# Performance work log

Measured on AMD Instinct MI355X. Metric: run time of the kernel, lower is better.

## Reference

```python
import jax, jax.numpy as jnp
import numpy as np

TEMPERATURE = 1.0
NUM_EXPERTS = 8


def setup_inputs() -> dict:
    key = jax.random.key(0)
    ks = jax.random.split(key, 7)
    B, S, H, E = 4, 4096, 1024, NUM_EXPERTS
    scale = 1.0 / np.sqrt(H)
    return {
        "hidden_states": jax.random.normal(ks[0], (B, S, H), dtype=jnp.float32),
        "w1": jax.random.normal(ks[1], (H, H // 2), dtype=jnp.float32) * scale,
        "b1": jax.random.normal(ks[2], (H // 2,), dtype=jnp.float32) * 0.01,
        "w2": jax.random.normal(ks[3], (H // 2, E), dtype=jnp.float32) * (1.0 / np.sqrt(H // 2)),
        "b2": jax.random.normal(ks[4], (E,), dtype=jnp.float32) * 0.01,
        "expert_W": jax.random.normal(ks[5], (E, H, H), dtype=jnp.float32) * scale,
        "expert_b": jax.random.normal(ks[6], (E, H), dtype=jnp.float32) * 0.01,
    }


def reference(hidden_states, w1, b1, w2, b2, expert_W, expert_b):
    # Router MLP: Linear(H, H//2) -> ReLU -> Linear(H//2, E)  (dropout inactive at eval)
    h = jax.nn.relu(jnp.einsum("bsh,hm->bsm", hidden_states, w1) + b1)
    routing_scores = (jnp.einsum("bsm,me->bse", h, w2) + b2) / TEMPERATURE
    expert_probs = jax.nn.softmax(routing_scores, axis=-1)
    # top-1 routing (topk with k=1 == argmax of probs)
    top_idx = jnp.argmax(expert_probs, axis=-1)  # [B, S]
    onehot = jax.nn.one_hot(top_idx, NUM_EXPERTS, dtype=hidden_states.dtype)  # [B, S, E]

    # _apply_expert_routing: for each expert, masked input -> dense transform -> masked accumulate
    routed = jnp.zeros_like(hidden_states)
    for e in range(NUM_EXPERTS):
        mask = onehot[..., e:e + 1]  # [B, S, 1]
        expert_out = jnp.einsum("bsh,hd->bsd", hidden_states * mask, expert_W[e]) + expert_b[e]
        routed = routed + expert_out * mask
    return routed
```

## Files before the change

### kernel.cpp

```cpp
#include <hip/hip_runtime.h>

#define NTOK 16384
#define HDIM 1024
#define MDIM 512
#define NEXP 8
#define CHUNK 128
#define MAXCHUNK 136
#define RCAP 4096
#define DELTA 0.02f
#define LSTR 72

typedef __bf16 bf16x8 __attribute__((ext_vector_type(8)));
typedef float floatx4 __attribute__((ext_vector_type(4)));

__global__ __launch_bounds__(256) void cvt_hs(
    const float* __restrict__ src, __bf16* __restrict__ dst)
{
  const size_t i = ((size_t)blockIdx.x * 256 + threadIdx.x) * 8;
  float4 a = *(const float4*)&src[i];
  float4 b = *(const float4*)&src[i + 4];
  bf16x8 o;
  o[0] = (__bf16)a.x; o[1] = (__bf16)a.y; o[2] = (__bf16)a.z; o[3] = (__bf16)a.w;
  o[4] = (__bf16)b.x; o[5] = (__bf16)b.y; o[6] = (__bf16)b.z; o[7] = (__bf16)b.w;
  *(bf16x8*)&dst[i] = o;
}

__global__ __launch_bounds__(256) void transpose_cvt(
    const float* __restrict__ src, __bf16* __restrict__ dst, int K, int C)
{
  __shared__ __align__(16) __bf16 T[64 * LSTR];
  const int b = blockIdx.z;
  const int k0 = blockIdx.x * 64, c0 = blockIdx.y * 64;
  const float* S = src + (size_t)b * K * C;
  __bf16* D = dst + (size_t)b * K * C;
  const int t = threadIdx.x;

  {
    const int r = t >> 2, cc = (t & 3) * 16;
    const float* p = S + (size_t)(k0 + r) * C + c0 + cc;
    float4 v0 = *(const float4*)&p[0];
    float4 v1 = *(const float4*)&p[4];
    float4 v2 = *(const float4*)&p[8];
    float4 v3 = *(const float4*)&p[12];
    float vv[16] = {v0.x, v0.y, v0.z, v0.w, v1.x, v1.y, v1.z, v1.w,
                    v2.x, v2.y, v2.z, v2.w, v3.x, v3.y, v3.z, v3.w};
#pragma unroll
    for (int j = 0; j < 16; ++j) T[(cc + j) * LSTR + r] = (__bf16)vv[j];
  }
  __syncthreads();
  {
    const int c = t >> 2, kk = (t & 3) * 16;
    __bf16* q = D + (size_t)(c0 + c) * K + k0 + kk;
    *(float4*)&q[0] = *(const float4*)&T[c * LSTR + kk];
    *(float4*)&q[8] = *(const float4*)&T[c * LSTR + kk + 8];
  }
}

__global__ __launch_bounds__(256) void gemm1_v2(
    const __bf16* __restrict__ A,
    const __bf16* __restrict__ Bt,
    const float* __restrict__ bias,
    float* __restrict__ Hout)
{
  __shared__ __align__(16) __bf16 As[128 * LSTR];
  __shared__ __align__(16) __bf16 Bs[128 * LSTR];

  const int tid = threadIdx.x;
  const int row0 = blockIdx.y * 128, col0 = blockIdx.x * 128;

  const int srow = tid >> 3;
  const int soff = (tid & 7) * 8;

  const __bf16* pa = A + (size_t)(row0 + srow) * HDIM + soff;
  const __bf16* pb = Bt + (size_t)(col0 + srow) * HDIM + soff;

  const int wave = tid >> 6, lane = tid & 63;
  const int wr = (wave >> 1) * 64, wc = (wave & 1) * 64;
  const int lrow = lane & 15, quad = lane >> 4;

  floatx4 acc[4][4];
#pragma unroll
  for (int i = 0; i < 4; ++i)
#pragma unroll
    for (int j = 0; j < 4; ++j) acc[i][j] = (floatx4){0.f, 0.f, 0.f, 0.f};

  for (int k0 = 0; k0 < HDIM; k0 += 64) {
#pragma unroll
    for (int p = 0; p < 4; ++p) {
      *(float4*)&As[(srow + p * 32) * LSTR + soff] =
          *(const float4*)&pa[(size_t)(p * 32) * HDIM + k0];
      *(float4*)&Bs[(srow + p * 32) * LSTR + soff] =
          *(const float4*)&pb[(size_t)(p * 32) * HDIM + k0];
    }
    __syncthreads();

#pragma unroll
    for (int kh = 0; kh < 2; ++kh) {
      bf16x8 a[4], b[4];
#pragma unroll
      for (int i = 0; i < 4; ++i)
        a[i] = *(const bf16x8*)&As[(wr + i * 16 + lrow) * LSTR + kh * 32 + quad * 8];
#pragma unroll
      for (int j = 0; j < 4; ++j)
        b[j] = *(const bf16x8*)&Bs[(wc + j * 16 + lrow) * LSTR + kh * 32 + quad * 8];
#pragma unroll
      for (int i = 0; i < 4; ++i)
#pragma unroll
        for (int j = 0; j < 4; ++j)
          acc[i][j] = __builtin_amdgcn_mfma_f32_16x16x32_bf16(a[i], b[j], acc[i][j], 0, 0, 0);
    }
    __syncthreads();
  }

#pragma unroll
  for (int i = 0; i < 4; ++i)
#pragma unroll
    for (int r = 0; r < 4; ++r) {
      const int row = row0 + wr + i * 16 + quad * 4 + r;
#pragma unroll
      for (int j = 0; j < 4; ++j) {
        const int col = col0 + wc + j * 16 + lrow;
        Hout[(size_t)row * MDIM + col] = fmaxf(acc[i][j][r] + bias[col], 0.f);
      }
    }
}

__global__ __launch_bounds__(256) void routing_flag(
    const float* __restrict__ Hq, const float* __restrict__ w2,
    const float* __restrict__ b2, int* __restrict__ top_idx,
    int* __restrict__ risky_n, int* __restrict__ risky)
{
  __shared__ int rbuf[4];
  __shared__ int rcnt;
  if (threadIdx.x == 0) rcnt = 0;
  __syncthreads();

  const int warp = threadIdx.x >> 6;
  const int lane = threadIdx.x & 63;
  const int t = blockIdx.x * 4 + warp;
  const float* hrow = Hq + (size_t)t * MDIM;

  float s[8] = {0, 0, 0, 0, 0, 0, 0, 0};
  for (int k = lane; k < MDIM; k += 64) {
    float hv = hrow[k];
    float4 wa = *(const float4*)&w2[k * 8];
    float4 wb = *(const float4*)&w2[k * 8 + 4];
    s[0] += hv * wa.x; s[1] += hv * wa.y; s[2] += hv * wa.z; s[3] += hv * wa.w;
    s[4] += hv * wb.x; s[5] += hv * wb.y; s[6] += hv * wb.z; s[7] += hv * wb.w;
  }
#pragma unroll
  for (int off = 32; off > 0; off >>= 1)
#pragma unroll
    for (int e = 0; e < 8; ++e) s[e] += __shfl_xor(s[e], off, 64);

  if (lane == 0) {
    float best = s[0] + b2[0], second = -1e30f;
    int bi = 0;
#pragma unroll
    for (int e = 1; e < 8; ++e) {
      float v = s[e] + b2[e];
      if (v > best) { second = best; best = v; bi = e; }
      else if (v > second) second = v;
    }
    top_idx[t] = bi;
    if (best - second < DELTA) {
      int slot = atomicAdd(&rcnt, 1);
      rbuf[slot] = t;
    }
  }
  __syncthreads();
  if (threadIdx.x == 0 && rcnt > 0) {
    int base = atomicAdd(risky_n, rcnt);
    for (int i = 0; i < rcnt; ++i)
      if (base + i < RCAP) risky[base + i] = rbuf[i];
  }
}

__global__ __launch_bounds__(256) void gemm1_fix_v2(
    const float* __restrict__ A,
    const float* __restrict__ W,
    const float* __restrict__ bias,
    const int* __restrict__ risky,
    float* __restrict__ Hout)
{
  __shared__ float As[32][33];
  __shared__ float Bs[32][64];
  __shared__ int toks[32];

  const int tid = threadIdx.x;
  if (tid < 32) toks[tid] = risky[blockIdx.y * 32 + tid];
  __syncthreads();
  if (toks[0] < 0) return;

  const int col0 = blockIdx.x * 64;
  const int tx = tid & 15, ty = tid >> 4;

  float acc0[4] = {0, 0, 0, 0}, acc1[4] = {0, 0, 0, 0};

  const int sr = tid >> 3;
  const int sc4 = (tid & 7) * 4;
  const int sc8 = (tid & 7) * 8;
  const int tokS = toks[sr];
  const float* pa = (tokS >= 0) ? A + (size_t)tokS * HDIM + sc4 : A;

  for (int k0 = 0; k0 < HDIM; k0 += 32) {
    float4 av = (tokS >= 0) ? *(const float4*)&pa[k0] : make_float4(0, 0, 0, 0);
    float4 b0 = *(const float4*)&W[(size_t)(k0 + sr) * MDIM + col0 + sc8];
    float4 b1v = *(const float4*)&W[(size_t)(k0 + sr) * MDIM + col0 + sc8 + 4];
    As[sc4 + 0][sr] = av.x; As[sc4 + 1][sr] = av.y;
    As[sc4 + 2][sr] = av.z; As[sc4 + 3][sr] = av.w;
    *(float4*)&Bs[sr][sc8] = b0;
    *(float4*)&Bs[sr][sc8 + 4] = b1v;
    __syncthreads();

#pragma unroll
    for (int k = 0; k < 32; ++k) {
      float a0 = As[k][ty], a1 = As[k][ty + 16];
      float4 bv = *(const float4*)&Bs[k][tx * 4];
      acc0[0] = fmaf(a0, bv.x, acc0[0]); acc0[1] = fmaf(a0, bv.y, acc0[1]);
      acc0[2] = fmaf(a0, bv.z, acc0[2]); acc0[3] = fmaf(a0, bv.w, acc0[3]);
      acc1[0] = fmaf(a1, bv.x, acc1[0]); acc1[1] = fmaf(a1, bv.y, acc1[1]);
      acc1[2] = fmaf(a1, bv.z, acc1[2]); acc1[3] = fmaf(a1, bv.w, acc1[3]);
    }
    __syncthreads();
  }

  const int c = col0 + tx * 4;
  const int t0 = toks[ty], t1 = toks[ty + 16];
  if (t0 >= 0) {
    float4 v;
    v.x = fmaxf(acc0[0] + bias[c + 0], 0.f); v.y = fmaxf(acc0[1] + bias[c + 1], 0.f);
    v.z = fmaxf(acc0[2] + bias[c + 2], 0.f); v.w = fmaxf(acc0[3] + bias[c + 3], 0.f);
    *(float4*)&Hout[(size_t)t0 * MDIM + c] = v;
  }
  if (t1 >= 0) {
    float4 v;
    v.x = fmaxf(acc1[0] + bias[c + 0], 0.f); v.y = fmaxf(acc1[1] + bias[c + 1], 0.f);
    v.z = fmaxf(acc1[2] + bias[c + 2], 0.f); v.w = fmaxf(acc1[3] + bias[c + 3], 0.f);
    *(float4*)&Hout[(size_t)t1 * MDIM + c] = v;
  }
}

__global__ __launch_bounds__(256) void rescore_fix(
    const float* __restrict__ Hq, const float* __restrict__ w2,
    const float* __restrict__ b2, const int* __restrict__ risky,
    int* __restrict__ top_idx)
{
  const int idx = blockIdx.x * 32 + (threadIdx.x >> 3);
  const int l8 = threadIdx.x & 7;
  const int t = risky[idx];

  float s[8] = {0, 0, 0, 0, 0, 0, 0, 0};
  if (t >= 0) {
    const float* hrow = Hq + (size_t)t * MDIM;
    for (int k = l8; k < MDIM; k += 8) {
      float hv = hrow[k];
      float4 wa = *(const float4*)&w2[k * 8];
      float4 wb = *(const float4*)&w2[k * 8 + 4];
      s[0] += hv * wa.x; s[1] += hv * wa.y; s[2] += hv * wa.z; s[3] += hv * wa.w;
      s[4] += hv * wb.x; s[5] += hv * wb.y; s[6] += hv * wb.z; s[7] += hv * wb.w;
    }
  }
#pragma unroll
  for (int off = 4; off > 0; off >>= 1)
#pragma unroll
    for (int e = 0; e < 8; ++e) s[e] += __shfl_xor(s[e], off, 64);

  if (l8 == 0 && t >= 0) {
    float best = s[0] + b2[0];
    int bi = 0;
#pragma unroll
    for (int e = 1; e < 8; ++e) {
      float v = s[e] + b2[e];
      if (v > best) { best = v; bi = e; }
    }
    top_idx[t] = bi;
  }
}

__global__ __launch_bounds__(256) void count_tokens(
    const int* __restrict__ top_idx, int* __restrict__ counts)
{
  __shared__ int lc[NEXP];
  if (threadIdx.x < NEXP) lc[threadIdx.x] = 0;
  __syncthreads();
  const int t = blockIdx.x * 256 + threadIdx.x;
  atomicAdd(&lc[top_idx[t]], 1);
  __syncthreads();
  if (threadIdx.x < NEXP) atomicAdd(&counts[threadIdx.x], lc[threadIdx.x]);
}

__global__ void make_offsets(const int* __restrict__ counts,
                             int* __restrict__ pad_off)
{
  if (threadIdx.x == 0) {
    int off = 0;
    for (int e = 0; e < NEXP; ++e) {
      pad_off[e] = off;
      off += ((counts[e] + CHUNK - 1) / CHUNK) * CHUNK;
    }
    pad_off[NEXP] = off;
  }
}

__global__ __launch_bounds__(256) void scatter_tokens(
    const int* __restrict__ top_idx, const int* __restrict__ pad_off,
    int* __restrict__ cursor, int* __restrict__ sorted)
{
  __shared__ int lc[NEXP];
  __shared__ int lbase[NEXP];
  if (threadIdx.x < NEXP) lc[threadIdx.x] = 0;
  __syncthreads();
  const int t = blockIdx.x * 256 + threadIdx.x;
  const int e = top_idx[t];
  const int r = atomicAdd(&lc[e], 1);
  __syncthreads();
  if (threadIdx.x < NEXP)
    lbase[threadIdx.x] = atomicAdd(&cursor[threadIdx.x], lc[threadIdx.x]);
  __syncthreads();
  sorted[pad_off[e] + lbase[e] + r] = t;
}

__global__ __launch_bounds__(256) void expert_gemm_v2(
    const __bf16* __restrict__ A,
    const __bf16* __restrict__ Wt,
    const float* __restrict__ Eb,
    const int* __restrict__ sorted,
    const int* __restrict__ top_idx,
    float* __restrict__ Out)
{
  __shared__ __align__(16) __bf16 As[128 * LSTR];
  __shared__ __align__(16) __bf16 Bs[128 * LSTR];
  __shared__ int toks[CHUNK];

  const int tid = threadIdx.x;
  if (tid < CHUNK) toks[tid] = sorted[(size_t)blockIdx.y * CHUNK + tid];
  __syncthreads();
  if (toks[0] < 0) return;

  const int e = top_idx[toks[0]];
  const int col0 = blockIdx.x * 128;

  const int srow = tid >> 3;
  const int soff = (tid & 7) * 8;

  const __bf16* pa[4];
#pragma unroll
  for (int p = 0; p < 4; ++p) {
    int tk = toks[srow + p * 32];
    pa[p] = A + (size_t)(tk >= 0 ? tk : 0) * HDIM + soff;
  }
  const __bf16* pb = Wt + ((size_t)e * HDIM + col0 + srow) * HDIM + soff;

  const int wave = tid >> 6, lane = tid & 63;
  const int wr = (wave >> 1) * 64, wc = (wave & 1) * 64;
  const int lrow = lane & 15, quad = lane >> 4;

  floatx4 acc[4][4];
#pragma unroll
  for (int i = 0; i < 4; ++i)
#pragma unroll
    for (int j = 0; j < 4; ++j) acc[i][j] = (floatx4){0.f, 0.f, 0.f, 0.f};

  for (int k0 = 0; k0 < HDIM; k0 += 64) {
#pragma unroll
    for (int p = 0; p < 4; ++p) {
      *(float4*)&As[(srow + p * 32) * LSTR + soff] = *(const float4*)&pa[p][k0];
      *(float4*)&Bs[(srow + p * 32) * LSTR + soff] =
          *(const float4*)&pb[(size_t)(p * 32) * HDIM + k0];
    }
    __syncthreads();

#pragma unroll
    for (int kh = 0; kh < 2; ++kh) {
      bf16x8 a[4], b[4];
#pragma unroll
      for (int i = 0; i < 4; ++i)
        a[i] = *(const bf16x8*)&As[(wr + i * 16 + lrow) * LSTR + kh * 32 + quad * 8];
#pragma unroll
      for (int j = 0; j < 4; ++j)
        b[j] = *(const bf16x8*)&Bs[(wc + j * 16 + lrow) * LSTR + kh * 32 + quad * 8];
#pragma unroll
      for (int i = 0; i < 4; ++i)
#pragma unroll
        for (int j = 0; j < 4; ++j)
          acc[i][j] = __builtin_amdgcn_mfma_f32_16x16x32_bf16(a[i], b[j], acc[i][j], 0, 0, 0);
    }
    __syncthreads();
  }

  const float* be = Eb + (size_t)e * HDIM + col0;
#pragma unroll
  for (int i = 0; i < 4; ++i)
#pragma unroll
    for (int r = 0; r < 4; ++r) {
      const int row = wr + i * 16 + quad * 4 + r;
      const int tok = toks[row];
      if (tok < 0) continue;
      float* po = Out + (size_t)tok * HDIM + col0;
#pragma unroll
      for (int j = 0; j < 4; ++j) {
        const int col = wc + j * 16 + lrow;
        po[col] = acc[i][j][r] + be[col];
      }
    }
}

extern "C" void kernel_launch(void* const* d_in, const int* in_sizes, int n_in,
                              void* d_out, int out_size, void* d_ws, size_t ws_size,
                              hipStream_t stream) {
  (void)in_sizes; (void)n_in; (void)out_size; (void)ws_size;

  const float* hs = (const float*)d_in[0];
  const float* w1 = (const float*)d_in[1];
  const float* b1 = (const float*)d_in[2];
  const float* w2 = (const float*)d_in[3];
  const float* b2 = (const float*)d_in[4];
  const float* eW = (const float*)d_in[5];
  const float* eb = (const float*)d_in[6];
  float* out = (float*)d_out;

  float* h = (float*)d_out;

  char* wsb = (char*)d_ws;
  int* top_idx = (int*)wsb;
  int* ctrl    = (int*)(wsb + 65536);
  int* counts  = ctrl;
  int* risky_n = ctrl + 8;
  int* cursor  = ctrl + 16;
  int* pad_off = (int*)(wsb + 65536 + 128);
  int* risky   = (int*)(wsb + 65792);
  int* sorted  = risky + RCAP;
  __bf16* hs_bf = (__bf16*)(wsb + 163840);
  __bf16* w1t   = (__bf16*)(wsb + 163840 + 33554432);
  __bf16* eWt   = (__bf16*)(wsb + 163840 + 33554432 + 1048576);

  hipMemsetAsync(ctrl, 0, 128, stream);
  hipMemsetAsync(risky, 0xFF, (RCAP + MAXCHUNK * CHUNK) * sizeof(int), stream);

  cvt_hs<<<NTOK * HDIM / (256 * 8), 256, 0, stream>>>(hs, hs_bf);
  transpose_cvt<<<dim3(HDIM / 64, MDIM / 64, 1), 256, 0, stream>>>(w1, w1t, HDIM, MDIM);
  transpose_cvt<<<dim3(HDIM / 64, HDIM / 64, NEXP), 256, 0, stream>>>(eW, eWt, HDIM, HDIM);

  gemm1_v2<<<dim3(MDIM / 128, NTOK / 128), 256, 0, stream>>>(hs_bf, w1t, b1, h);
  routing_flag<<<NTOK / 4, 256, 0, stream>>>(h, w2, b2, top_idx, risky_n, risky);
  gemm1_fix_v2<<<dim3(MDIM / 64, RCAP / 32), 256, 0, stream>>>(hs, w1, b1, risky, h);
  rescore_fix<<<RCAP / 32, 256, 0, stream>>>(h, w2, b2, risky, top_idx);
  count_tokens<<<NTOK / 256, 256, 0, stream>>>(top_idx, counts);
  make_offsets<<<1, 64, 0, stream>>>(counts, pad_off);
  scatter_tokens<<<NTOK / 256, 256, 0, stream>>>(top_idx, pad_off, cursor, sorted);
  expert_gemm_v2<<<dim3(HDIM / 128, MAXCHUNK), 256, 0, stream>>>(hs_bf, eWt, eb, sorted, top_idx, out);
}
```

Measured before the change: 340.6 us.

## Fuse router score into GEMM1 epilogue and use direct global-to-LDS swizzled loads

Router GEMM1 now computes the second linear layer (w2 projection) in its epilogue and writes per-column-block partial scores, so the 16384x512 hidden activation is no longer stored and reread. A separate argmax kernel reduces the partial scores and flags near-tie tokens. Recomputed hidden rows for flagged tokens go to a compact buffer. Both bf16 GEMMs switch to global_load_lds 16-byte loads with an XOR-swizzled unpadded LDS layout to cut VGPR staging and bank conflicts. make_offsets is folded into scatter_tokens, removing one launch. The fused epilogue adds shuffle reductions and an extra LDS pass.

```diff
diff --git a/kernel.cpp b/kernel.cpp
--- a/kernel.cpp
+++ b/kernel.cpp
@@ -13,6 +13,12 @@
 typedef __bf16 bf16x8 __attribute__((ext_vector_type(8)));
 typedef float floatx4 __attribute__((ext_vector_type(4)));
 
+__device__ __forceinline__ void gll16(const void* g, void* l) {
+  __builtin_amdgcn_global_load_lds(
+      (const __attribute__((address_space(1))) void*)g,
+      (__attribute__((address_space(3))) void*)l, 16, 0, 0);
+}
+
 __global__ __launch_bounds__(256) void cvt_hs(
     const float* __restrict__ src, __bf16* __restrict__ dst)
 {
@@ -34,7 +40,6 @@
   const float* S = src + (size_t)b * K * C;
   __bf16* D = dst + (size_t)b * K * C;
   const int t = threadIdx.x;
-
   {
     const int r = t >> 2, cc = (t & 3) * 16;
     const float* p = S + (size_t)(k0 + r) * C + c0 + cc;
@@ -56,28 +61,32 @@
   }
 }
 
-__global__ __launch_bounds__(256) void gemm1_v2(
+__global__ __launch_bounds__(256) void gemm1_score(
     const __bf16* __restrict__ A,
     const __bf16* __restrict__ Bt,
     const float* __restrict__ bias,
-    float* __restrict__ Hout)
-{
-  __shared__ __align__(16) __bf16 As[128 * LSTR];
-  __shared__ __align__(16) __bf16 Bs[128 * LSTR];
+    const float* __restrict__ w2,
+    float* __restrict__ scores_part)
+{
+  __shared__ __align__(16) __bf16 As[128 * 64];
+  __shared__ __align__(16) __bf16 Bs[128 * 64];
 
   const int tid = threadIdx.x;
   const int row0 = blockIdx.y * 128, col0 = blockIdx.x * 128;
-
-  const int srow = tid >> 3;
-  const int soff = (tid & 7) * 8;
-
-  const __bf16* pa = A + (size_t)(row0 + srow) * HDIM + soff;
-  const __bf16* pb = Bt + (size_t)(col0 + srow) * HDIM + soff;
-
   const int wave = tid >> 6, lane = tid & 63;
+  const int lrow8 = lane >> 3;
+  const int gchunk = (lane & 7) ^ lrow8;
   const int wr = (wave >> 1) * 64, wc = (wave & 1) * 64;
   const int lrow = lane & 15, quad = lane >> 4;
 
+  const __bf16 *pa[4], *pb[4];
+#pragma unroll
+  for (int p = 0; p < 4; ++p) {
+    const int rb = wave * 8 + p * 32;
+    pa[p] = A + (size_t)(row0 + rb + lrow8) * HDIM + gchunk * 8;
+    pb[p] = Bt + (size_t)(col0 + rb + lrow8) * HDIM + gchunk * 8;
+  }
+
   floatx4 acc[4][4];
 #pragma unroll
   for (int i = 0; i < 4; ++i)
@@ -87,22 +96,22 @@
   for (int k0 = 0; k0 < HDIM; k0 += 64) {
 #pragma unroll
     for (int p = 0; p < 4; ++p) {
-      *(float4*)&As[(srow + p * 32) * LSTR + soff] =
-          *(const float4*)&pa[(size_t)(p * 32) * HDIM + k0];
-      *(float4*)&Bs[(srow + p * 32) * LSTR + soff] =
-          *(const float4*)&pb[(size_t)(p * 32) * HDIM + k0];
-    }
-    __syncthreads();
-
+      const int rb = wave * 8 + p * 32;
+      gll16(pa[p] + k0, &As[rb * 64]);
+      gll16(pb[p] + k0, &Bs[rb * 64]);
+    }
+    __syncthreads();
 #pragma unroll
     for (int kh = 0; kh < 2; ++kh) {
       bf16x8 a[4], b[4];
 #pragma unroll
       for (int i = 0; i < 4; ++i)
-        a[i] = *(const bf16x8*)&As[(wr + i * 16 + lrow) * LSTR + kh * 32 + quad * 8];
+        a[i] = *(const bf16x8*)&As[(wr + i * 16 + lrow) * 64 +
+                                   (((kh * 4 + quad) ^ (lrow & 7)) * 8)];
 #pragma unroll
       for (int j = 0; j < 4; ++j)
-        b[j] = *(const bf16x8*)&Bs[(wc + j * 16 + lrow) * LSTR + kh * 32 + quad * 8];
+        b[j] = *(const bf16x8*)&Bs[(wc + j * 16 + lrow) * 64 +
+                                   (((kh * 4 + quad) ^ (lrow & 7)) * 8)];
 #pragma unroll
       for (int i = 0; i < 4; ++i)
 #pragma unroll
@@ -112,76 +121,101 @@
     __syncthreads();
   }
 
-#pragma unroll
-  for (int i = 0; i < 4; ++i)
+  float* w2s = (float*)As;
+  float* sblk = (float*)Bs;
+  *(float4*)&w2s[tid * 4] = *(const float4*)&w2[col0 * 8 + tid * 4];
+  __syncthreads();
+
+  float bj[4];
+  float4 wja[4], wjb[4];
+#pragma unroll
+  for (int j = 0; j < 4; ++j) {
+    const int cl = wc + j * 16 + lrow;
+    bj[j] = bias[col0 + cl];
+    wja[j] = *(const float4*)&w2s[cl * 8];
+    wjb[j] = *(const float4*)&w2s[cl * 8 + 4];
+  }
+
+#pragma unroll
+  for (int i = 0; i < 4; ++i) {
 #pragma unroll
     for (int r = 0; r < 4; ++r) {
-      const int row = row0 + wr + i * 16 + quad * 4 + r;
+      float4 sA = {0, 0, 0, 0}, sB = {0, 0, 0, 0};
 #pragma unroll
       for (int j = 0; j < 4; ++j) {
-        const int col = col0 + wc + j * 16 + lrow;
-        Hout[(size_t)row * MDIM + col] = fmaxf(acc[i][j][r] + bias[col], 0.f);
+        float h = fmaxf(acc[i][j][r] + bj[j], 0.f);
+        sA.x += h * wja[j].x; sA.y += h * wja[j].y;
+        sA.z += h * wja[j].z; sA.w += h * wja[j].w;
+        sB.x += h * wjb[j].x; sB.y += h * wjb[j].y;
+        sB.z += h * wjb[j].z; sB.w += h * wjb[j].w;
       }
-    }
-}
-
-__global__ __launch_bounds__(256) void routing_flag(
-    const float* __restrict__ Hq, const float* __restrict__ w2,
-    const float* __restrict__ b2, int* __restrict__ top_idx,
-    int* __restrict__ risky_n, int* __restrict__ risky)
-{
-  __shared__ int rbuf[4];
-  __shared__ int rcnt;
+#pragma unroll
+      for (int m = 1; m <= 8; m <<= 1) {
+        sA.x += __shfl_xor(sA.x, m, 64); sA.y += __shfl_xor(sA.y, m, 64);
+        sA.z += __shfl_xor(sA.z, m, 64); sA.w += __shfl_xor(sA.w, m, 64);
+        sB.x += __shfl_xor(sB.x, m, 64); sB.y += __shfl_xor(sB.y, m, 64);
+        sB.z += __shfl_xor(sB.z, m, 64); sB.w += __shfl_xor(sB.w, m, 64);
+      }
+      if (lrow == 0) {
+        const int rloc = wr + i * 16 + quad * 4 + r;
+        *(float4*)&sblk[((wave & 1) * 128 + rloc) * 8] = sA;
+        *(float4*)&sblk[((wave & 1) * 128 + rloc) * 8 + 4] = sB;
+      }
+    }
+  }
+  __syncthreads();
+  {
+    const int r = tid >> 1, e4 = (tid & 1) * 4;
+    float4 v0 = *(const float4*)&sblk[r * 8 + e4];
+    float4 v1 = *(const float4*)&sblk[(128 + r) * 8 + e4];
+    float4 o = {v0.x + v1.x, v0.y + v1.y, v0.z + v1.z, v0.w + v1.w};
+    *(float4*)&scores_part[((size_t)blockIdx.x * NTOK + row0 + r) * 8 + e4] = o;
+  }
+}
+
+__global__ __launch_bounds__(256) void routing_argmax(
+    const float* __restrict__ scores_part, const float* __restrict__ b2,
+    int* __restrict__ top_idx, int* __restrict__ risky_n,
+    int* __restrict__ risky)
+{
+  __shared__ int rbuf[256];
+  __shared__ int rcnt, rbase;
   if (threadIdx.x == 0) rcnt = 0;
   __syncthreads();
 
-  const int warp = threadIdx.x >> 6;
-  const int lane = threadIdx.x & 63;
-  const int t = blockIdx.x * 4 + warp;
-  const float* hrow = Hq + (size_t)t * MDIM;
-
-  float s[8] = {0, 0, 0, 0, 0, 0, 0, 0};
-  for (int k = lane; k < MDIM; k += 64) {
-    float hv = hrow[k];
-    float4 wa = *(const float4*)&w2[k * 8];
-    float4 wb = *(const float4*)&w2[k * 8 + 4];
-    s[0] += hv * wa.x; s[1] += hv * wa.y; s[2] += hv * wa.z; s[3] += hv * wa.w;
-    s[4] += hv * wb.x; s[5] += hv * wb.y; s[6] += hv * wb.z; s[7] += hv * wb.w;
-  }
-#pragma unroll
-  for (int off = 32; off > 0; off >>= 1)
-#pragma unroll
-    for (int e = 0; e < 8; ++e) s[e] += __shfl_xor(s[e], off, 64);
-
-  if (lane == 0) {
-    float best = s[0] + b2[0], second = -1e30f;
-    int bi = 0;
-#pragma unroll
-    for (int e = 1; e < 8; ++e) {
-      float v = s[e] + b2[e];
-      if (v > best) { second = best; best = v; bi = e; }
-      else if (v > second) second = v;
-    }
-    top_idx[t] = bi;
-    if (best - second < DELTA) {
-      int slot = atomicAdd(&rcnt, 1);
-      rbuf[slot] = t;
-    }
-  }
-  __syncthreads();
-  if (threadIdx.x == 0 && rcnt > 0) {
-    int base = atomicAdd(risky_n, rcnt);
-    for (int i = 0; i < rcnt; ++i)
-      if (base + i < RCAP) risky[base + i] = rbuf[i];
+  const int t = blockIdx.x * 256 + threadIdx.x;
+  float4 sa = {0, 0, 0, 0}, sb = {0, 0, 0, 0};
+#pragma unroll
+  for (int c = 0; c < 4; ++c) {
+    float4 va = *(const float4*)&scores_part[((size_t)c * NTOK + t) * 8];
+    float4 vb = *(const float4*)&scores_part[((size_t)c * NTOK + t) * 8 + 4];
+    sa.x += va.x; sa.y += va.y; sa.z += va.z; sa.w += va.w;
+    sb.x += vb.x; sb.y += vb.y; sb.z += vb.z; sb.w += vb.w;
+  }
+  float s[8] = {sa.x + b2[0], sa.y + b2[1], sa.z + b2[2], sa.w + b2[3],
+                sb.x + b2[4], sb.y + b2[5], sb.z + b2[6], sb.w + b2[7]};
+  float best = s[0], second = -1e30f;
+  int bi = 0;
+#pragma unroll
+  for (int e = 1; e < 8; ++e) {
+    if (s[e] > best) { second = best; best = s[e]; bi = e; }
+    else if (s[e] > second) second = s[e];
+  }
+  top_idx[t] = bi;
+  if (best - second < DELTA) rbuf[atomicAdd(&rcnt, 1)] = t;
+  __syncthreads();
+  if (threadIdx.x == 0 && rcnt > 0) rbase = atomicAdd(risky_n, rcnt);
+  __syncthreads();
+  if ((int)threadIdx.x < rcnt) {
+    int slot = rbase + threadIdx.x;
+    if (slot < RCAP) risky[slot] = rbuf[threadIdx.x];
   }
 }
 
 __global__ __launch_bounds__(256) void gemm1_fix_v2(
-    const float* __restrict__ A,
-    const float* __restrict__ W,
-    const float* __restrict__ bias,
-    const int* __restrict__ risky,
-    float* __restrict__ Hout)
+    const float* __restrict__ A, const float* __restrict__ W,
+    const float* __restrict__ bias, const int* __restrict__ risky,
+    float* __restrict__ hfix)
 {
   __shared__ float As[32][33];
   __shared__ float Bs[32][64];
@@ -194,21 +228,24 @@
 
   const int col0 = blockIdx.x * 64;
   const int tx = tid & 15, ty = tid >> 4;
-
   float acc0[4] = {0, 0, 0, 0}, acc1[4] = {0, 0, 0, 0};
 
   const int sr = tid >> 3;
-  const int sc4 = (tid & 7) * 4;
-  const int sc8 = (tid & 7) * 8;
+  const int sc4 = (tid & 3) * 8;
+  const int lo = tid & 7;
+  const int sc8 = lo * 8;
   const int tokS = toks[sr];
-  const float* pa = (tokS >= 0) ? A + (size_t)tokS * HDIM + sc4 : A;
+  const float* pa = (tokS >= 0) ? A + (size_t)tokS * HDIM : A;
 
   for (int k0 = 0; k0 < HDIM; k0 += 32) {
-    float4 av = (tokS >= 0) ? *(const float4*)&pa[k0] : make_float4(0, 0, 0, 0);
+    float4 av = make_float4(0, 0, 0, 0);
+    if (tokS >= 0) av = *(const float4*)&pa[k0 + (lo & 3) * 4 + (lo >> 2) * 16];
     float4 b0 = *(const float4*)&W[(size_t)(k0 + sr) * MDIM + col0 + sc8];
     float4 b1v = *(const float4*)&W[(size_t)(k0 + sr) * MDIM + col0 + sc8 + 4];
-    As[sc4 + 0][sr] = av.x; As[sc4 + 1][sr] = av.y;
-    As[sc4 + 2][sr] = av.z; As[sc4 + 3][sr] = av.w;
+    const int kk = (lo & 3) * 4 + (lo >> 2) * 16;
+    As[kk + 0][sr] = av.x; As[kk + 1][sr] = av.y;
+    As[kk + 2][sr] = av.z; As[kk + 3][sr] = av.w;
+    (void)sc4;
     *(float4*)&Bs[sr][sc8] = b0;
     *(float4*)&Bs[sr][sc8 + 4] = b1v;
     __syncthreads();
@@ -226,23 +263,23 @@
   }
 
   const int c = col0 + tx * 4;
-  const int t0 = toks[ty], t1 = toks[ty + 16];
-  if (t0 >= 0) {
+  const int i0 = blockIdx.y * 32 + ty, i1 = blockIdx.y * 32 + ty + 16;
+  if (toks[ty] >= 0) {
     float4 v;
     v.x = fmaxf(acc0[0] + bias[c + 0], 0.f); v.y = fmaxf(acc0[1] + bias[c + 1], 0.f);
     v.z = fmaxf(acc0[2] + bias[c + 2], 0.f); v.w = fmaxf(acc0[3] + bias[c + 3], 0.f);
-    *(float4*)&Hout[(size_t)t0 * MDIM + c] = v;
-  }
-  if (t1 >= 0) {
+    *(float4*)&hfix[(size_t)i0 * MDIM + c] = v;
+  }
+  if (toks[ty + 16] >= 0) {
     float4 v;
     v.x = fmaxf(acc1[0] + bias[c + 0], 0.f); v.y = fmaxf(acc1[1] + bias[c + 1], 0.f);
     v.z = fmaxf(acc1[2] + bias[c + 2], 0.f); v.w = fmaxf(acc1[3] + bias[c + 3], 0.f);
-    *(float4*)&Hout[(size_t)t1 * MDIM + c] = v;
+    *(float4*)&hfix[(size_t)i1 * MDIM + c] = v;
   }
 }
 
 __global__ __launch_bounds__(256) void rescore_fix(
-    const float* __restrict__ Hq, const float* __restrict__ w2,
+    const float* __restrict__ hfix, const float* __restrict__ w2,
     const float* __restrict__ b2, const int* __restrict__ risky,
     int* __restrict__ top_idx)
 {
@@ -252,7 +289,7 @@
 
   float s[8] = {0, 0, 0, 0, 0, 0, 0, 0};
   if (t >= 0) {
-    const float* hrow = Hq + (size_t)t * MDIM;
+    const float* hrow = hfix + (size_t)idx * MDIM;
     for (int k = l8; k < MDIM; k += 8) {
       float hv = hrow[k];
       float4 wa = *(const float4*)&w2[k * 8];
@@ -284,32 +321,24 @@
   __shared__ int lc[NEXP];
   if (threadIdx.x < NEXP) lc[threadIdx.x] = 0;
   __syncthreads();
-  const int t = blockIdx.x * 256 + threadIdx.x;
-  atomicAdd(&lc[top_idx[t]], 1);
+  atomicAdd(&lc[top_idx[blockIdx.x * 256 + threadIdx.x]], 1);
   __syncthreads();
   if (threadIdx.x < NEXP) atomicAdd(&counts[threadIdx.x], lc[threadIdx.x]);
 }
 
-__global__ void make_offsets(const int* __restrict__ counts,
-                             int* __restrict__ pad_off)
-{
+__global__ __launch_bounds__(256) void scatter_tokens(
+    const int* __restrict__ top_idx, const int* __restrict__ counts,
+    int* __restrict__ cursor, int* __restrict__ sorted)
+{
+  __shared__ int lc[NEXP], lbase[NEXP], off_s[NEXP];
+  if (threadIdx.x < NEXP) lc[threadIdx.x] = 0;
   if (threadIdx.x == 0) {
     int off = 0;
     for (int e = 0; e < NEXP; ++e) {
-      pad_off[e] = off;
+      off_s[e] = off;
       off += ((counts[e] + CHUNK - 1) / CHUNK) * CHUNK;
     }
-    pad_off[NEXP] = off;
-  }
-}
-
-__global__ __launch_bounds__(256) void scatter_tokens(
-    const int* __restrict__ top_idx, const int* __restrict__ pad_off,
-    int* __restrict__ cursor, int* __restrict__ sorted)
-{
-  __shared__ int lc[NEXP];
-  __shared__ int lbase[NEXP];
-  if (threadIdx.x < NEXP) lc[threadIdx.x] = 0;
+  }
   __syncthreads();
   const int t = blockIdx.x * 256 + threadIdx.x;
   const int e = top_idx[t];
@@ -318,10 +347,10 @@
   if (threadIdx.x < NEXP)
     lbase[threadIdx.x] = atomicAdd(&cursor[threadIdx.x], lc[threadIdx.x]);
   __syncthreads();
-  sorted[pad_off[e] + lbase[e] + r] = t;
-}
-
-__global__ __launch_bounds__(256) void expert_gemm_v2(
+  sorted[off_s[e] + lbase[e] + r] = t;
+}
+
+__global__ __launch_bounds__(256) void expert_gemm_v3(
     const __bf16* __restrict__ A,
     const __bf16* __restrict__ Wt,
     const float* __restrict__ Eb,
@@ -329,8 +358,8 @@
     const int* __restrict__ top_idx,
     float* __restrict__ Out)
 {
-  __shared__ __align__(16) __bf16 As[128 * LSTR];
-  __shared__ __align__(16) __bf16 Bs[128 * LSTR];
+  __shared__ __align__(16) __bf16 As[128 * 64];
+  __shared__ __align__(16) __bf16 Bs[128 * 64];
   __shared__ int toks[CHUNK];
 
   const int tid = threadIdx.x;
@@ -340,22 +369,21 @@
 
   const int e = top_idx[toks[0]];
   const int col0 = blockIdx.x * 128;
-
-  const int srow = tid >> 3;
-  const int soff = (tid & 7) * 8;
-
-  const __bf16* pa[4];
-#pragma unroll
-  for (int p = 0; p < 4; ++p) {
-    int tk = toks[srow + p * 32];
-    pa[p] = A + (size_t)(tk >= 0 ? tk : 0) * HDIM + soff;
-  }
-  const __bf16* pb = Wt + ((size_t)e * HDIM + col0 + srow) * HDIM + soff;
-
   const int wave = tid >> 6, lane = tid & 63;
+  const int lrow8 = lane >> 3;
+  const int gchunk = (lane & 7) ^ lrow8;
   const int wr = (wave >> 1) * 64, wc = (wave & 1) * 64;
   const int lrow = lane & 15, quad = lane >> 4;
 
+  const __bf16 *pa[4], *pb[4];
+#pragma unroll
+  for (int p = 0; p < 4; ++p) {
+    const int rb = wave * 8 + p * 32;
+    const int tk = toks[rb + lrow8];
+    pa[p] = A + (size_t)(tk < 0 ? 0 : tk) * HDIM + gchunk * 8;
+    pb[p] = Wt + ((size_t)e * HDIM + col0 + rb + lrow8) * HDIM + gchunk * 8;
+  }
+
   floatx4 acc[4][4];
 #pragma unroll
   for (int i = 0; i < 4; ++i)
@@ -365,21 +393,22 @@
   for (int k0 = 0; k0 < HDIM; k0 += 64) {
 #pragma unroll
     for (int p = 0; p < 4; ++p) {
-      *(float4*)&As[(srow + p * 32) * LSTR + soff] = *(const float4*)&pa[p][k0];
-      *(float4*)&Bs[(srow + p * 32) * LSTR + soff] =
-          *(const float4*)&pb[(size_t)(p * 32) * HDIM + k0];
-    }
-    __syncthreads();
-
+      const int rb = wave * 8 + p * 32;
+      gll16(pa[p] + k0, &As[rb * 64]);
+      gll16(pb[p] + k0, &Bs[rb * 64]);
+    }
+    __syncthreads();
 #pragma unroll
     for (int kh = 0; kh < 2; ++kh) {
       bf16x8 a[4], b[4];
 #pragma unroll
       for (int i = 0; i < 4; ++i)
-        a[i] = *(const bf16x8*)&As[(wr + i * 16 + lrow) * LSTR + kh * 32 + quad * 8];
+        a[i] = *(const bf16x8*)&As[(wr + i * 16 + lrow) * 64 +
+                                   (((kh * 4 + quad) ^ (lrow & 7)) * 8)];
 #pragma unroll
       for (int j = 0; j < 4; ++j)
-        b[j] = *(const bf16x8*)&Bs[(wc + j * 16 + lrow) * LSTR + kh * 32 + quad * 8];
+        b[j] = *(const bf16x8*)&Bs[(wc + j * 16 + lrow) * 64 +
+                                   (((kh * 4 + quad) ^ (lrow & 7)) * 8)];
 #pragma unroll
       for (int i = 0; i < 4; ++i)
 #pragma unroll
@@ -420,7 +449,8 @@
   const float* eb = (const float*)d_in[6];
   float* out = (float*)d_out;
 
-  float* h = (float*)d_out;
+  float* hfix = (float*)d_out;
+  float* scores_part = hfix + (size_t)RCAP * MDIM;
 
   char* wsb = (char*)d_ws;
   int* top_idx = (int*)wsb;
@@ -428,7 +458,6 @@
   int* counts  = ctrl;
   int* risky_n = ctrl + 8;
   int* cursor  = ctrl + 16;
-  int* pad_off = (int*)(wsb + 65536 + 128);
   int* risky   = (int*)(wsb + 65792);
   int* sorted  = risky + RCAP;
   __bf16* hs_bf = (__bf16*)(wsb + 163840);
@@ -442,12 +471,11 @@
   transpose_cvt<<<dim3(HDIM / 64, MDIM / 64, 1), 256, 0, stream>>>(w1, w1t, HDIM, MDIM);
   transpose_cvt<<<dim3(HDIM / 64, HDIM / 64, NEXP), 256, 0, stream>>>(eW, eWt, HDIM, HDIM);
 
-  gemm1_v2<<<dim3(MDIM / 128, NTOK / 128), 256, 0, stream>>>(hs_bf, w1t, b1, h);
-  routing_flag<<<NTOK / 4, 256, 0, stream>>>(h, w2, b2, top_idx, risky_n, risky);
-  gemm1_fix_v2<<<dim3(MDIM / 64, RCAP / 32), 256, 0, stream>>>(hs, w1, b1, risky, h);
-  rescore_fix<<<RCAP / 32, 256, 0, stream>>>(h, w2, b2, risky, top_idx);
+  gemm1_score<<<dim3(MDIM / 128, NTOK / 128), 256, 0, stream>>>(hs_bf, w1t, b1, w2, scores_part);
+  routing_argmax<<<NTOK / 256, 256, 0, stream>>>(scores_part, b2, top_idx, risky_n, risky);
+  gemm1_fix_v2<<<dim3(MDIM / 64, RCAP / 32), 256, 0, stream>>>(hs, w1, b1, risky, hfix);
+  rescore_fix<<<RCAP / 32, 256, 0, stream>>>(hfix, w2, b2, risky, top_idx);
   count_tokens<<<NTOK / 256, 256, 0, stream>>>(top_idx, counts);
-  make_offsets<<<1, 64, 0, stream>>>(counts, pad_off);
-  scatter_tokens<<<NTOK / 256, 256, 0, stream>>>(top_idx, pad_off, cursor, sorted);
-  expert_gemm_v2<<<dim3(HDIM / 128, MAXCHUNK), 256, 0, stream>>>(hs_bf, eWt, eb, sorted, top_idx, out);
-}
+  scatter_tokens<<<NTOK / 256, 256, 0, stream>>>(top_idx, counts, cursor, sorted);
+  expert_gemm_v3<<<dim3(HDIM / 128, MAXCHUNK), 256, 0, stream>>>(hs_bf, eWt, eb, sorted, top_idx, out);
+}
```

After: 331.7 us. -2.6%, faster.
